# Performance work log

Measured on AMD Instinct MI355X. Metric: run time of the kernel, lower is better.

## Reference

```python
import jax, jax.numpy as jnp
import numpy as np

H = 16  # num_heads


def setup_inputs() -> dict:
    key = jax.random.key(0)
    ks = jax.random.split(key, 9)
    L, N, E, I = 2048, 2, 2048, 2048
    s = 0.02
    return {
        "query": jax.random.normal(ks[0], (L, N, E), jnp.float32),
        "q_proj": jax.random.normal(ks[1], (I, E), jnp.float32) * s,
        "q_bias": jax.random.normal(ks[2], (I,), jnp.float32) * s,
        "k_proj": jax.random.normal(ks[3], (I, E), jnp.float32) * s,
        "k_bias": jax.random.normal(ks[4], (I,), jnp.float32) * s,
        "v_proj": jax.random.normal(ks[5], (I, E), jnp.float32) * s,
        "v_bias": jax.random.normal(ks[6], (I,), jnp.float32) * s,
        "out_proj": jax.random.normal(ks[7], (E, I), jnp.float32) * s,
        "out_bias": jax.random.normal(ks[8], (E,), jnp.float32) * s,
    }


def reference(query, q_proj, q_bias, k_proj, k_bias, v_proj, v_bias, out_proj, out_bias):
    L, N, E = query.shape
    h = H
    d = q_proj.shape[0] // h
    scale = d ** (-0.5)

    def split_heads(x):
        # [L, N, h*d] -> [N, h, L, d]  (matches view(L, N*h, d).transpose(0,1))
        return x.reshape(L, N, h, d).transpose(1, 2, 0, 3)

    q = split_heads(query @ q_proj.T + q_bias) * scale
    k = split_heads(query @ k_proj.T + k_bias)
    v = split_heads(query @ v_proj.T + v_bias)

    scores = jnp.einsum('nhld,nhkd->nhlk', q, k)  # [N, h, L, L]
    causal = jnp.tril(jnp.ones((L, L), dtype=bool))
    scores = jnp.where(causal, scores, jnp.float32(-10000.0))
    attn = jax.nn.softmax(scores, axis=-1)
    # dropout_p = 0.0 -> identity
    ctx = jnp.einsum('nhlk,nhkd->nhld', attn, v)
    ctx = ctx.transpose(2, 0, 1, 3).reshape(L, N, h * d)  # [L, N, h*d]
    return ctx @ out_proj.T + out_bias  # [L, N, E]
```

## Files before the change

### kernel.cpp

```cpp
#include <hip/hip_runtime.h>
#include <stdint.h>

#define L_SEQ 2048
#define NB 2
#define EMB 2048
#define II 2048
#define NH 16
#define DH 128
#define MROWS (L_SEQ * NB)

typedef __attribute__((ext_vector_type(8))) short bf16x8;
typedef __attribute__((ext_vector_type(4))) float f32x4;
typedef unsigned short u16;
typedef unsigned int u32;

__device__ __forceinline__ u16 f2bf(float f) {
  u32 u = __builtin_bit_cast(u32, f);
  u = u + 0x7fffu + ((u >> 16) & 1u);
  return (u16)(u >> 16);
}
__device__ __forceinline__ u16 f2bf_trunc(float f) {
  return (u16)(__builtin_bit_cast(u32, f) >> 16);
}

__device__ __forceinline__ void gl_lds16(const void* g, const u16* l) {
  __builtin_amdgcn_global_load_lds(
      (const __attribute__((address_space(1))) void*)(uintptr_t)g,
      (__attribute__((address_space(3))) void*)(u32)(uintptr_t)l, 16, 0, 0);
}

__global__ __launch_bounds__(256) void cast_all(
    const float* __restrict__ q, const float* __restrict__ w0, const float* __restrict__ w1,
    const float* __restrict__ w2, const float* __restrict__ w3, u16* __restrict__ dq,
    u16* __restrict__ dw) {
  const int b = blockIdx.x, t = threadIdx.x;
  const float* src;
  u16* dst;
  int idx;
  if (b < 8192) {
    src = q; dst = dq; idx = b * 256 + t;
  } else {
    int u = b - 8192;
    int sel = u >> 12;
    src = (sel == 0) ? w0 : (sel == 1) ? w1 : (sel == 2) ? w2 : w3;
    dst = dw + (size_t)sel * II * EMB;
    idx = (u & 4095) * 256 + t;
  }
  float4 v = ((const float4*)src)[idx];
  ushort4 o;
  o.x = f2bf(v.x); o.y = f2bf(v.y); o.z = f2bf(v.z); o.w = f2bf(v.w);
  ((ushort4*)dst)[idx] = o;
}

__global__ __launch_bounds__(256) void transpose_v(const u16* __restrict__ V,
                                                   u16* __restrict__ Vt) {
  __shared__ u16 tile[128][72];
  const int lb = blockIdx.x * 64;
  const int h = blockIdx.y;
  const u16* src = V + (size_t)h * L_SEQ * DH;
  u16* dst = Vt + (size_t)h * DH * L_SEQ;
  const int t = threadIdx.x;
  {
    const int l = t & 63, d0 = (t >> 6) * 32;
#pragma unroll
    for (int c = 0; c < 4; c++) {
      uint4 u = *(const uint4*)(src + (size_t)(lb + l) * DH + d0 + c * 8);
      const u16* e = (const u16*)&u;
#pragma unroll
      for (int x = 0; x < 8; x++) tile[d0 + c * 8 + x][l] = e[x];
    }
  }
  __syncthreads();
  {
    const int d = t >> 1, lc = (t & 1) * 32;
#pragma unroll
    for (int c = 0; c < 4; c++) {
      uint4 u = *(const uint4*)&tile[d][lc + c * 8];
      *(uint4*)(dst + (size_t)d * L_SEQ + lb + lc + c * 8) = u;
    }
  }
}

#define BK8 64
#define NT8 (EMB / BK8)

__global__ __launch_bounds__(512, 2) void gemm_qkv_8p(
    const u16* __restrict__ A, const u16* __restrict__ B, const float* __restrict__ qb,
    const float* __restrict__ kb, const float* __restrict__ vb, u16* __restrict__ out_bf,
    float qscale) {
  __shared__ __align__(16) u16 sm[2][32768];
  const int t = threadIdx.x;
  const int lane = t & 63, wv = t >> 6;
  const int quad = lane >> 4, l15 = lane & 15, x7 = l15 & 7;
  const int wm2 = wv >> 2, wn4 = wv & 3;
  const int srow = lane >> 3;
  const int schunk = (lane & 7) ^ (lane >> 3);

  const int bid = blockIdx.x;
  const int swz = (bid & 7) * 48 + (bid >> 3);
  const int bxx = swz >> 4;
  const int byy = swz & 15;
  const int n0 = bxx * 256, m0 = byy * 256;

  const u16* abase = A + (size_t)m0 * EMB;
  const u16* bbase = B + (size_t)n0 * EMB;

  auto stageA = [&](int buf, int k0, int u) {
    int row = u * 64 + wv * 8 + srow;
    const u16* dst = (buf ? sm[1] : sm[0]) + u * 4096 + wv * 512;
    gl_lds16(abase + (size_t)row * EMB + k0 + schunk * 8, dst);
  };
  auto stageB = [&](int buf, int k0, int u) {
    int row = u * 64 + wv * 8 + srow;
    const u16* dst = (buf ? sm[1] : sm[0]) + 16384 + u * 4096 + wv * 512;
    gl_lds16(bbase + (size_t)row * EMB + k0 + schunk * 8, dst);
  };

  stageA(0, 0, 0); stageA(0, 0, 2);
  stageB(0, 0, 0); stageB(0, 0, 1); stageB(0, 0, 2); stageB(0, 0, 3);
  stageA(0, 0, 1); stageA(0, 0, 3);
  stageA(1, BK8, 0); stageA(1, BK8, 2);
  __asm__ volatile("s_waitcnt vmcnt(4)" ::: "memory");
  __builtin_amdgcn_s_barrier();

  f32x4 acc[8][4] = {};
  bf16x8 afr[4][2];

#pragma unroll 1
  for (int tt = 0; tt < NT8; ++tt) {
    const int cb = tt & 1, nb_ = (tt + 1) & 1;
    const u16* cur = cb ? sm[1] : sm[0];
    const int kn1 = (tt + 1) * BK8;
    const int kn2 = (tt + 2) * BK8;
    const bool pf1 = (tt + 1 < NT8);
    const bool pf2 = (tt + 2 < NT8);

    {
#pragma unroll
      for (int mi = 0; mi < 4; mi++)
#pragma unroll
        for (int ks = 0; ks < 2; ks++)
          afr[mi][ks] =
              *(const bf16x8*)(cur + (wm2 * 128 + mi * 16 + l15) * 64 + (((ks * 4 + quad) ^ x7)) * 8);
      bf16x8 bfr2[2][2];
#pragma unroll
      for (int nj = 0; nj < 2; nj++)
#pragma unroll
        for (int ks = 0; ks < 2; ks++)
          bfr2[nj][ks] = *(const bf16x8*)(cur + 16384 + (wn4 * 64 + nj * 16 + l15) * 64 +
                                          (((ks * 4 + quad) ^ x7)) * 8);
      if (pf1) { stageB(nb_, kn1, 0); stageB(nb_, kn1, 1); stageB(nb_, kn1, 2); stageB(nb_, kn1, 3); }
      __builtin_amdgcn_s_barrier();
      __builtin_amdgcn_s_setprio(1);
#pragma unroll
      for (int ks = 0; ks < 2; ks++)
#pragma unroll
        for (int mi = 0; mi < 4; mi++)
#pragma unroll
          for (int nj = 0; nj < 2; nj++)
            acc[mi][nj] =
                __builtin_amdgcn_mfma_f32_16x16x32_bf16(afr[mi][ks], bfr2[nj][ks], acc[mi][nj], 0, 0, 0);
      __builtin_amdgcn_s_setprio(0);
      __builtin_amdgcn_s_barrier();
    }

    {
      bf16x8 bfr2[2][2];
#pragma unroll
      for (int nj = 0; nj < 2; nj++)
#pragma unroll
        for (int ks = 0; ks < 2; ks++)
          bfr2[nj][ks] = *(const bf16x8*)(cur + 16384 + (wn4 * 64 + (nj + 2) * 16 + l15) * 64 +
                                          (((ks * 4 + quad) ^ x7)) * 8);
      if (pf1) {
        stageA(nb_, kn1, 1); stageA(nb_, kn1, 3);
        __asm__ volatile("s_waitcnt vmcnt(8)" ::: "memory");
      } else {
        __asm__ volatile("s_waitcnt vmcnt(0)" ::: "memory");
      }
      __builtin_amdgcn_s_barrier();
      __builtin_amdgcn_s_setprio(1);
#pragma unroll
      for (int ks = 0; ks < 2; ks++)
#pragma unroll
        for (int mi = 0; mi < 4; mi++)
#pragma unroll
          for (int nj = 0; nj < 2; nj++)
            acc[mi][nj + 2] =
                __builtin_amdgcn_mfma_f32_16x16x32_bf16(afr[mi][ks], bfr2[nj][ks], acc[mi][nj + 2], 0, 0, 0);
      __builtin_amdgcn_s_setprio(0);
      __builtin_amdgcn_s_barrier();
    }

    {
#pragma unroll
      for (int mi = 0; mi < 4; mi++)
#pragma unroll
        for (int ks = 0; ks < 2; ks++)
          afr[mi][ks] = *(const bf16x8*)(cur + (wm2 * 128 + (mi + 4) * 16 + l15) * 64 +
                                         (((ks * 4 + quad) ^ x7)) * 8);
      bf16x8 bfr2[2][2];
#pragma unroll
      for (int nj = 0; nj < 2; nj++)
#pragma unroll
        for (int ks = 0; ks < 2; ks++)
          bfr2[nj][ks] = *(const bf16x8*)(cur + 16384 + (wn4 * 64 + nj * 16 + l15) * 64 +
                                          (((ks * 4 + quad) ^ x7)) * 8);
      if (pf2) { stageA(cb, kn2, 0); stageA(cb, kn2, 2); }
      __builtin_amdgcn_s_barrier();
      __builtin_amdgcn_s_setprio(1);
#pragma unroll
      for (int ks = 0; ks < 2; ks++)
#pragma unroll
        for (int mi = 0; mi < 4; mi++)
#pragma unroll
          for (int nj = 0; nj < 2; nj++)
            acc[mi + 4][nj] =
                __builtin_amdgcn_mfma_f32_16x16x32_bf16(afr[mi][ks], bfr2[nj][ks], acc[mi + 4][nj], 0, 0, 0);
      __builtin_amdgcn_s_setprio(0);
      __builtin_amdgcn_s_barrier();
    }

    {
      bf16x8 bfr2[2][2];
#pragma unroll
      for (int nj = 0; nj < 2; nj++)
#pragma unroll
        for (int ks = 0; ks < 2; ks++)
          bfr2[nj][ks] = *(const bf16x8*)(cur + 16384 + (wn4 * 64 + (nj + 2) * 16 + l15) * 64 +
                                          (((ks * 4 + quad) ^ x7)) * 8);
      if (pf2) {
        __asm__ volatile("s_waitcnt vmcnt(4)" ::: "memory");
      } else if (pf1) {
        __asm__ volatile("s_waitcnt vmcnt(2)" ::: "memory");
      }
      __builtin_amdgcn_s_barrier();
      __builtin_amdgcn_s_setprio(1);
#pragma unroll
      for (int ks = 0; ks < 2; ks++)
#pragma unroll
        for (int mi = 0; mi < 4; mi++)
#pragma unroll
          for (int nj = 0; nj < 2; nj++)
            acc[mi + 4][nj + 2] =
                __builtin_amdgcn_mfma_f32_16x16x32_bf16(afr[mi][ks], bfr2[nj][ks], acc[mi + 4][nj + 2], 0, 0, 0);
      __builtin_amdgcn_s_setprio(0);
      __builtin_amdgcn_s_barrier();
    }
  }

  const int mat = n0 >> 11;
  const float* bp = (mat == 0) ? qb : (mat == 1) ? kb : vb;
  const float sc2 = (mat == 0) ? qscale : 1.0f;
#pragma unroll
  for (int mi = 0; mi < 8; mi++) {
#pragma unroll
    for (int nj = 0; nj < 4; nj++) {
#pragma unroll
      for (int r = 0; r < 4; r++) {
        int row = m0 + wm2 * 128 + mi * 16 + quad * 4 + r;
        int col = n0 + wn4 * 64 + nj * 16 + l15;
        int cc = col & 2047;
        float v = (acc[mi][nj][r] + bp[cc]) * sc2;
        int l = row >> 1, nb = row & 1;
        int hh = cc >> 7, dd = cc & 127;
        out_bf[(size_t)mat * MROWS * II + ((size_t)(nb * NH + hh) * L_SEQ + l) * DH + dd] =
            f2bf(v);
      }
    }
  }
}

__global__ __launch_bounds__(256) void gemm_nt(
    const u16* __restrict__ A, const u16* __restrict__ B, const float* __restrict__ b0,
    const float* __restrict__ b1, const float* __restrict__ b2, u16* __restrict__ out_bf,
    float* __restrict__ out_f, int Nd, int K, float qscale, int mode) {
  __shared__ __align__(16) u16 a_sm[128 * 64];
  __shared__ __align__(16) u16 b_sm[128 * 64];
  const int t = threadIdx.x;
  const int lane = t & 63, wv = t >> 6;
  const int quad = lane >> 4, l15 = lane & 15;
  const int x7 = l15 & 7;
  const int wm = (wv >> 1) * 64, wn = (wv & 1) * 64;
  const int m0 = blockIdx.y * 128, n0 = blockIdx.x * 128;
  const int srow = lane >> 3;
  const int schunk = (lane & 7) ^ (lane >> 3);

  f32x4 acc[4][4] = {};
  const u16* abase = A + (size_t)m0 * K;
  const u16* bbase = B + (size_t)n0 * K;

  for (int k0 = 0; k0 < K; k0 += 64) {
    __syncthreads();
#pragma unroll
    for (int j = 0; j < 4; j++) {
      int ci = wv * 4 + j;
      int row = ci * 8 + srow;
      gl_lds16(abase + (size_t)row * K + k0 + schunk * 8, a_sm + ci * 512);
      gl_lds16(bbase + (size_t)row * K + k0 + schunk * 8, b_sm + ci * 512);
    }
    __syncthreads();
#pragma unroll
    for (int ks = 0; ks < 2; ks++) {
      bf16x8 af[4], bfr[4];
#pragma unroll
      for (int i = 0; i < 4; i++)
        af[i] = *(const bf16x8*)(a_sm + (wm + i * 16 + l15) * 64 + ((ks * 4 + quad) ^ x7) * 8);
#pragma unroll
      for (int j = 0; j < 4; j++)
        bfr[j] = *(const bf16x8*)(b_sm + (wn + j * 16 + l15) * 64 + ((ks * 4 + quad) ^ x7) * 8);
#pragma unroll
      for (int i = 0; i < 4; i++)
#pragma unroll
        for (int j = 0; j < 4; j++)
          acc[i][j] = __builtin_amdgcn_mfma_f32_16x16x32_bf16(af[i], bfr[j], acc[i][j], 0, 0, 0);
    }
  }

  const int mat = n0 >> 11;
  const float* bp = (mode == 1) ? b0 : (mat == 0 ? b0 : (mat == 1 ? b1 : b2));
  const float sc2 = (mode == 0 && mat == 0) ? qscale : 1.0f;
#pragma unroll
  for (int i = 0; i < 4; i++) {
#pragma unroll
    for (int j = 0; j < 4; j++) {
#pragma unroll
      for (int r = 0; r < 4; r++) {
        int row = m0 + wm + i * 16 + quad * 4 + r;
        int col = n0 + wn + j * 16 + l15;
        if (mode == 0) {
          int cc = col & 2047;
          float v = (acc[i][j][r] + bp[cc]) * sc2;
          int l = row >> 1, nb = row & 1;
          int hh = cc >> 7, dd = cc & 127;
          out_bf[(size_t)mat * MROWS * II + ((size_t)(nb * NH + hh) * L_SEQ + l) * DH + dd] =
              f2bf(v);
        } else {
          out_f[(size_t)row * Nd + col] = acc[i][j][r] + bp[col];
        }
      }
    }
  }
}

__global__ __launch_bounds__(256, 2) void flash_attn(
    const u16* __restrict__ Qh, const u16* __restrict__ Kh, const u16* __restrict__ Vt,
    u16* __restrict__ ctx) {
  __shared__ __align__(16) u16 k_sm[128 * 128];
  __shared__ __align__(16) u16 v_sm[128 * 128];
  const int bx = blockIdx.x;
  const int nh = ((bx & 7) << 2) | ((bx >> 3) & 3);
  const int g = (bx >> 5) & 7;
  const int qt = (bx < 256) ? (15 - g) : g;
  const int q0 = qt * 128;
  const int nK = qt + 1;
  const int t = threadIdx.x;
  const int lane = t & 63, wv = t >> 6;
  const int quad = lane >> 4, l15 = lane & 15;
  const int x7 = l15 & 7;
  const size_t hq = (size_t)nh * L_SEQ * DH;
  const u16* qp = Qh + hq;
  const u16* kp = Kh + hq;
  const u16* vp = Vt + hq;
  const int n = nh >> 4, h = nh & 15;
  const int srow = lane >> 4;
  const int spos = lane & 15;
  u16* pw = k_sm + wv * 4096;

  bf16x8 qf[2][4];
#pragma unroll
  for (int mi = 0; mi < 2; mi++)
#pragma unroll
    for (int ks = 0; ks < 4; ks++)
      qf[mi][ks] = *(const bf16x8*)(qp + (size_t)(q0 + wv * 32 + mi * 16 + l15) * DH +
                                    ks * 32 + quad * 8);

  f32x4 o_acc[2][8] = {};
  float l_part[2][4] = {};

#pragma unroll 1
  for (int jb = 0; jb < nK; jb++) {
    const int kb = jb * 128;
    __syncthreads();
#pragma unroll
    for (int i = 0; i < 8; i++) {
      int ci = wv * 8 + i;
      int row = ci * 4 + srow;
      int gc = spos ^ (row & 7);
      gl_lds16(kp + (size_t)(kb + row) * DH + gc * 8, k_sm + ci * 512);
      gl_lds16(vp + (size_t)row * L_SEQ + kb + gc * 8, v_sm + ci * 512);
    }
    __syncthreads();

    f32x4 s[2][8] = {};
    __builtin_amdgcn_s_setprio(1);
#pragma unroll
    for (int nt = 0; nt < 8; nt++) {
#pragma unroll
      for (int ks = 0; ks < 4; ks++) {
        bf16x8 kf = *(const bf16x8*)(k_sm + (nt * 16 + l15) * 128 + ((ks * 4 + quad) ^ x7) * 8);
#pragma unroll
        for (int mi = 0; mi < 2; mi++)
          s[mi][nt] = __builtin_amdgcn_mfma_f32_16x16x32_bf16(qf[mi][ks], kf, s[mi][nt], 0, 0, 0);
      }
    }
    __builtin_amdgcn_s_setprio(0);
    __syncthreads();

    const bool diag = (jb == qt);
#pragma unroll
    for (int mi = 0; mi < 2; mi++) {
      const int rowg = q0 + wv * 32 + mi * 16 + quad * 4;
#pragma unroll
      for (int nt = 0; nt < 8; nt++) {
        const int colg = kb + nt * 16 + l15;
#pragma unroll
        for (int r = 0; r < 4; r++) {
          float p = __builtin_amdgcn_exp2f(s[mi][nt][r]);
          if (diag && colg > rowg + r) p = 0.f;
          l_part[mi][r] += p;
          int pr = mi * 16 + quad * 4 + r;
          int chunk = nt * 2 + (l15 >> 3);
          int pos = chunk ^ (pr & 7);
          pw[pr * 128 + pos * 8 + (l15 & 7)] = f2bf_trunc(p);
        }
      }
    }
    __asm__ volatile("s_waitcnt lgkmcnt(0)" ::: "memory");

    bf16x8 pf[2][4];
#pragma unroll
    for (int mi = 0; mi < 2; mi++)
#pragma unroll
      for (int ks = 0; ks < 4; ks++)
        pf[mi][ks] = *(const bf16x8*)(pw + (mi * 16 + l15) * 128 + ((ks * 4 + quad) ^ x7) * 8);
    __builtin_amdgcn_s_setprio(1);
#pragma unroll
    for (int nt = 0; nt < 8; nt++) {
#pragma unroll
      for (int ks = 0; ks < 4; ks++) {
        bf16x8 vf = *(const bf16x8*)(v_sm + (nt * 16 + l15) * 128 + ((ks * 4 + quad) ^ x7) * 8);
#pragma unroll
        for (int mi = 0; mi < 2; mi++)
          o_acc[mi][nt] =
              __builtin_amdgcn_mfma_f32_16x16x32_bf16(pf[mi][ks], vf, o_acc[mi][nt], 0, 0, 0);
      }
    }
    __builtin_amdgcn_s_setprio(0);
  }

#pragma unroll
  for (int mi = 0; mi < 2; mi++) {
#pragma unroll
    for (int r = 0; r < 4; r++) {
      float lv = l_part[mi][r];
#pragma unroll
      for (int off = 1; off < 16; off <<= 1) lv += __shfl_xor(lv, off, 64);
      float inv = 1.f / lv;
      const int lrow = q0 + wv * 32 + mi * 16 + quad * 4 + r;
#pragma unroll
      for (int nt = 0; nt < 8; nt++) {
        int dd = nt * 16 + l15;
        ctx[((size_t)lrow * NB + n) * EMB + h * DH + dd] = f2bf(o_acc[mi][nt][r] * inv);
      }
    }
  }
}

extern "C" void kernel_launch(void* const* d_in, const int* in_sizes, int n_in,
                              void* d_out, int out_size, void* d_ws, size_t ws_size,
                              hipStream_t stream) {
  const float* query    = (const float*)d_in[0];
  const float* q_proj   = (const float*)d_in[1];
  const float* q_bias   = (const float*)d_in[2];
  const float* k_proj   = (const float*)d_in[3];
  const float* k_bias   = (const float*)d_in[4];
  const float* v_proj   = (const float*)d_in[5];
  const float* v_bias   = (const float*)d_in[6];
  const float* out_proj = (const float*)d_in[7];
  const float* out_bias = (const float*)d_in[8];

  u16* ws  = (u16*)d_ws;
  u16* Xbf = ws;
  u16* Wq  = Xbf + (size_t)MROWS * EMB;
  u16* Wk  = Wq + (size_t)II * EMB;
  u16* Wv  = Wk + (size_t)II * EMB;
  u16* Wo  = Wv + (size_t)II * EMB;
  u16* Qw  = Wo + (size_t)EMB * II;
  u16* Kw  = Qw + (size_t)MROWS * II;
  u16* Vw  = Kw + (size_t)MROWS * II;
  u16* Cw  = Vw + (size_t)MROWS * II;
  u16* Vtb = Xbf;

  cast_all<<<8192 + 4 * 4096, 256, 0, stream>>>(query, q_proj, k_proj, v_proj, out_proj,
                                                Xbf, Wq);

  const float qscale = 0.08838834764831845f * 1.4426950408889634f;
  gemm_qkv_8p<<<384, 512, 0, stream>>>(Xbf, Wq, q_bias, k_bias, v_bias, Qw, qscale);

  transpose_v<<<dim3(L_SEQ / 64, NB * NH), 256, 0, stream>>>(Vw, Vtb);

  flash_attn<<<512, 256, 0, stream>>>(Qw, Kw, Vtb, Cw);

  gemm_nt<<<dim3(EMB / 128, MROWS / 128), 256, 0, stream>>>(
      Cw, Wo, out_bias, nullptr, nullptr, nullptr, (float*)d_out, EMB, II, 1.0f, 1);
}
```

Baseline: 447.0 us.

## Double-buffer flash-attention K/V tiles at 64-key granularity with prefetch

The causal flash-attention loop now works on 64-key K/V tiles instead of 128-key tiles. It keeps two LDS buffers and issues the global-to-LDS load for the next tile before computing on the current one. The goal is to overlap K/V memory traffic with the QK^T and PV MFMA work, and to replace one of the per-iteration __syncthreads with a lighter s_barrier. The trade-off is twice as many loop iterations, with more barrier and softmax-store overhead per key processed. The diagonal mask now covers the last two half-tiles.

New measurement: 400.6 us. 10.4% less time.

```diff
diff --git a/kernel.cpp b/kernel.cpp
--- a/kernel.cpp
+++ b/kernel.cpp
@@ -346,14 +346,14 @@
 __global__ __launch_bounds__(256, 2) void flash_attn(
     const u16* __restrict__ Qh, const u16* __restrict__ Kh, const u16* __restrict__ Vt,
     u16* __restrict__ ctx) {
-  __shared__ __align__(16) u16 k_sm[128 * 128];
-  __shared__ __align__(16) u16 v_sm[128 * 128];
+  __shared__ __align__(16) u16 k_sm[2][64 * 128];
+  __shared__ __align__(16) u16 v_sm[2][128 * 64];
   const int bx = blockIdx.x;
   const int nh = ((bx & 7) << 2) | ((bx >> 3) & 3);
   const int g = (bx >> 5) & 7;
   const int qt = (bx < 256) ? (15 - g) : g;
   const int q0 = qt * 128;
-  const int nK = qt + 1;
+  const int nK = 2 * (qt + 1);
   const int t = threadIdx.x;
   const int lane = t & 63, wv = t >> 6;
   const int quad = lane >> 4, l15 = lane & 15;
@@ -365,7 +365,23 @@
   const int n = nh >> 4, h = nh & 15;
   const int srow = lane >> 4;
   const int spos = lane & 15;
-  u16* pw = k_sm + wv * 4096;
+  const int vrow = lane >> 3;
+  const int vpos = lane & 7;
+
+  auto stageKV = [&](int bb, int kb) {
+#pragma unroll
+    for (int i = 0; i < 4; i++) {
+      int ci = wv * 4 + i;
+      int krow = ci * 4 + srow;
+      int gck = spos ^ (krow & 7);
+      gl_lds16(kp + (size_t)(kb + krow) * DH + gck * 8,
+               (bb ? k_sm[1] : k_sm[0]) + ci * 512);
+      int drow = ci * 8 + vrow;
+      int gcv = vpos ^ (drow & 7);
+      gl_lds16(vp + (size_t)drow * L_SEQ + kb + gcv * 8,
+               (bb ? v_sm[1] : v_sm[0]) + ci * 512);
+    }
+  };
 
   bf16x8 qf[2][4];
 #pragma unroll
@@ -378,41 +394,44 @@
   f32x4 o_acc[2][8] = {};
   float l_part[2][4] = {};
 
+  stageKV(0, 0);
+
 #pragma unroll 1
   for (int jb = 0; jb < nK; jb++) {
-    const int kb = jb * 128;
+    const int b = jb & 1;
+    const u16* kbuf = b ? k_sm[1] : k_sm[0];
+    const u16* vbuf = b ? v_sm[1] : v_sm[0];
+    u16* pwb = (b ? k_sm[1] : k_sm[0]) + wv * 2048;
+    const int kb = jb * 64;
+
     __syncthreads();
-#pragma unroll
-    for (int i = 0; i < 8; i++) {
-      int ci = wv * 8 + i;
-      int row = ci * 4 + srow;
-      int gc = spos ^ (row & 7);
-      gl_lds16(kp + (size_t)(kb + row) * DH + gc * 8, k_sm + ci * 512);
-      gl_lds16(vp + (size_t)row * L_SEQ + kb + gc * 8, v_sm + ci * 512);
-    }
-    __syncthreads();
-
-    f32x4 s[2][8] = {};
+    if (jb + 1 < nK) stageKV(b ^ 1, kb + 64);
+
+    f32x4 s[2][4] = {};
     __builtin_amdgcn_s_setprio(1);
 #pragma unroll
-    for (int nt = 0; nt < 8; nt++) {
+    for (int nt = 0; nt < 4; nt++) {
 #pragma unroll
       for (int ks = 0; ks < 4; ks++) {
-        bf16x8 kf = *(const bf16x8*)(k_sm + (nt * 16 + l15) * 128 + ((ks * 4 + quad) ^ x7) * 8);
+        bf16x8 kf = *(const bf16x8*)(kbuf + (nt * 16 + l15) * 128 + ((ks * 4 + quad) ^ x7) * 8);
 #pragma unroll
         for (int mi = 0; mi < 2; mi++)
           s[mi][nt] = __builtin_amdgcn_mfma_f32_16x16x32_bf16(qf[mi][ks], kf, s[mi][nt], 0, 0, 0);
       }
     }
     __builtin_amdgcn_s_setprio(0);
-    __syncthreads();
-
-    const bool diag = (jb == qt);
+
+    __asm__ volatile("s_waitcnt lgkmcnt(0)" ::: "memory");
+    __builtin_amdgcn_sched_barrier(0);
+    __builtin_amdgcn_s_barrier();
+    __builtin_amdgcn_sched_barrier(0);
+
+    const bool diag = (jb >= nK - 2);
 #pragma unroll
     for (int mi = 0; mi < 2; mi++) {
       const int rowg = q0 + wv * 32 + mi * 16 + quad * 4;
 #pragma unroll
-      for (int nt = 0; nt < 8; nt++) {
+      for (int nt = 0; nt < 4; nt++) {
         const int colg = kb + nt * 16 + l15;
 #pragma unroll
         for (int r = 0; r < 4; r++) {
@@ -422,24 +441,25 @@
           int pr = mi * 16 + quad * 4 + r;
           int chunk = nt * 2 + (l15 >> 3);
           int pos = chunk ^ (pr & 7);
-          pw[pr * 128 + pos * 8 + (l15 & 7)] = f2bf_trunc(p);
+          pwb[pr * 64 + pos * 8 + (l15 & 7)] = f2bf_trunc(p);
         }
       }
     }
     __asm__ volatile("s_waitcnt lgkmcnt(0)" ::: "memory");
-
-    bf16x8 pf[2][4];
+    __builtin_amdgcn_sched_barrier(0);
+
+    bf16x8 pf[2][2];
 #pragma unroll
     for (int mi = 0; mi < 2; mi++)
 #pragma unroll
-      for (int ks = 0; ks < 4; ks++)
-        pf[mi][ks] = *(const bf16x8*)(pw + (mi * 16 + l15) * 128 + ((ks * 4 + quad) ^ x7) * 8);
+      for (int ks = 0; ks < 2; ks++)
+        pf[mi][ks] = *(const bf16x8*)(pwb + (mi * 16 + l15) * 64 + ((ks * 4 + quad) ^ x7) * 8);
     __builtin_amdgcn_s_setprio(1);
 #pragma unroll
     for (int nt = 0; nt < 8; nt++) {
 #pragma unroll
-      for (int ks = 0; ks < 4; ks++) {
-        bf16x8 vf = *(const bf16x8*)(v_sm + (nt * 16 + l15) * 128 + ((ks * 4 + quad) ^ x7) * 8);
+      for (int ks = 0; ks < 2; ks++) {
+        bf16x8 vf = *(const bf16x8*)(vbuf + (nt * 16 + l15) * 64 + ((ks * 4 + quad) ^ x7) * 8);
 #pragma unroll
         for (int mi = 0; mi < 2; mi++)
           o_acc[mi][nt] =
```
